# Kernel optimization log

Measured on AMD Instinct MI355X. Metric: run time of the kernel, lower is better.

## Reference

```python
import jax, jax.numpy as jnp
import numpy as np

N = 10000        # nodes
E = 160000       # edges (avg degree 16)
MUL = 128        # channel multiplicity
A = 10           # node-attr (species one-hot) dim
RAD = 8          # radial bessel features
INV_SQRT3 = 0.5773502691896258  # CG coefficient for 1o x 1o -> 0e


def _mlp(x, Ws):
    # RadialMLP: linear layers with SiLU between, no activation on last
    for W in Ws[:-1]:
        x = jax.nn.silu(x @ W)
    return x @ Ws[-1]


def setup_inputs() -> dict:
    key = jax.random.key(0)
    ks = jax.random.split(key, 25)

    def g(k, shape):
        return jax.random.normal(k, shape, jnp.float32) / np.float32(np.sqrt(shape[0]))

    return {
        "node_attrs": jax.random.uniform(ks[0], (N, A), jnp.float32),
        "node_feats": jax.random.normal(ks[1], (N, 4 * MUL), jnp.float32),
        "edge_attrs": jax.random.normal(ks[2], (E, 4), jnp.float32),
        "edge_feats": jax.random.uniform(ks[3], (E, RAD), jnp.float32),
        "W_src": g(ks[5], (A, MUL)),
        "W_tgt": g(ks[6], (A, MUL)),
        "W_up0": g(ks[7], (MUL, MUL)),
        "W_up1": g(ks[8], (MUL, MUL)),
        "W_skip0": g(ks[9], (MUL, MUL)),
        "W_skip1": g(ks[10], (MUL, MUL)),
        "W_res0": g(ks[11], (MUL, 2 * MUL)),
        "W_res1": g(ks[12], (MUL, MUL)),
        "W_lin1_0": g(ks[13], (2 * MUL, 2 * MUL)),
        "W_lin1_1": g(ks[14], (2 * MUL, MUL)),
        "W_lin2_0": g(ks[15], (MUL, MUL)),
        "W_lin2_1": g(ks[16], (MUL, MUL)),
        "W_rad1": g(ks[17], (RAD + 2 * MUL, 64)),
        "W_rad2": g(ks[18], (64, 64)),
        "W_rad3": g(ks[19], (64, 64)),
        "W_rad4": g(ks[20], (64, 4 * MUL)),
        "W_den1": g(ks[21], (RAD + 2 * MUL, 64)),
        "W_den2": g(ks[22], (64, 1)),
        "alpha": jnp.ones((), jnp.float32),   # scaled by 20 inside (alpha = param * 20)
        "beta": jnp.zeros((), jnp.float32),
        "edge_index": jax.random.randint(ks[4], (E, 2), 0, N),
    }


def _forward(node_attrs, node_feats, edge_attrs, edge_feats,
             W_src, W_tgt, W_up0, W_up1, W_skip0, W_skip1, W_res0, W_res1,
             W_lin1_0, W_lin1_1, W_lin2_0, W_lin2_1,
             W_rad1, W_rad2, W_rad3, W_rad4, W_den1, W_den2,
             alpha, beta, edge_index):
    n = node_feats.shape[0]
    # split node feats into 128x0e scalars and 128x1o vectors (mul_ir layout)
    s = node_feats[:, :MUL]                           # [N, 128]
    v = node_feats[:, MUL:].reshape(n, MUL, 3)        # [N, 128, 3]

    # skip connection: Linear(node_feats_irreps -> hidden_irreps)
    sc_s = s @ W_skip0
    sc_v = jnp.einsum("nui,uv->nvi", v, W_skip1)
    sc = jnp.concatenate([sc_s, sc_v.reshape(n, -1)], axis=-1)  # [N, 512]

    # linear_up (node_feats -> edge_irreps) and linear_res (-> irreps_nonlin)
    up_s = s @ W_up0
    up_v = jnp.einsum("nui,uv->nvi", v, W_up1)
    res_s = s @ W_res0                                # [N, 256] (scalars + gates)
    res_v = jnp.einsum("nui,uv->nvi", v, W_res1)      # [N, 128, 3]

    # per-species scalar embeddings, gathered per edge
    src_emb = node_attrs @ W_src                      # [N, 128]
    tgt_emb = node_attrs @ W_tgt
    snd = edge_index[:, 0]
    rcv = edge_index[:, 1]
    aug = jnp.concatenate([edge_feats, src_emb[snd], tgt_emb[rcv]], axis=-1)  # [E, 264]

    # radial MLP -> per-edge tensor-product weights; density MLP
    tpw = _mlp(aug, [W_rad1, W_rad2, W_rad3, W_rad4])  # [E, 512]
    edge_density = jnp.tanh(_mlp(aug, [W_den1, W_den2]) ** 2)  # [E, 1]
    density = jax.ops.segment_sum(edge_density, rcv, num_segments=n)  # [N, 1]

    # equivariant tensor product (uvu, per-edge weights), lmax=1 CG paths
    xs = up_s[snd]                                    # [E, 128]
    xv = up_v[snd]                                    # [E, 128, 3]
    y0 = edge_attrs[:, :1]                            # [E, 1]
    y1 = edge_attrs[:, 1:4]                           # [E, 3]
    wA, wB, wC, wD = jnp.split(tpw, 4, axis=-1)
    mA = wA * xs * y0                                               # 0e x 0e -> 0e
    mD = wD * jnp.einsum("eui,ei->eu", xv, y1) * INV_SQRT3          # 1o x 1o -> 0e
    mB = (wB * xs)[:, :, None] * y1[:, None, :]                     # 0e x 1o -> 1o
    mC = wC[:, :, None] * xv * y0[:, :, None]                       # 1o x 0e -> 1o
    m_s = jnp.concatenate([mA, mD], axis=-1)          # [E, 256]
    m_v = jnp.concatenate([mB, mC], axis=1)           # [E, 256, 3]

    # scatter-add messages to receiver nodes
    msg_s = jax.ops.segment_sum(m_s, rcv, num_segments=n)  # [N, 256]
    msg_v = jax.ops.segment_sum(m_v, rcv, num_segments=n)  # [N, 256, 3]

    # linear_1 (irreps_mid -> irreps_nonlin), density normalization, residual
    msg_s = msg_s @ W_lin1_0                          # [N, 256]
    msg_v = jnp.einsum("nui,uv->nvi", msg_v, W_lin1_1)  # [N, 128, 3]
    denom = density * beta + alpha * 20.0             # [N, 1]
    msg_s = msg_s / denom + res_s
    msg_v = msg_v / denom[..., None] + res_v

    # equivariant gate nonlinearity: silu on scalars, sigmoid gates on vectors
    scal = jax.nn.silu(msg_s[:, :MUL])
    gate = jax.nn.sigmoid(msg_s[:, MUL:])
    vec = msg_v * gate[:, :, None]

    # linear_2 and reshape to [N, channels, (lmax+1)^2]
    out_s = scal @ W_lin2_0                           # [N, 128]
    out_v = jnp.einsum("nui,uv->nvi", vec, W_lin2_1)  # [N, 128, 3]
    message = jnp.concatenate([out_s[:, :, None], out_v], axis=-1)  # [N, 128, 4]
    return message, sc


def reference(node_attrs, node_feats, edge_attrs, edge_feats,
              W_src, W_tgt, W_up0, W_up1, W_skip0, W_skip1, W_res0, W_res1,
              W_lin1_0, W_lin1_1, W_lin2_0, W_lin2_1,
              W_rad1, W_rad2, W_rad3, W_rad4, W_den1, W_den2,
              alpha, beta, edge_index):
    return _forward(node_attrs, node_feats, edge_attrs, edge_feats,
                    W_src, W_tgt, W_up0, W_up1, W_skip0, W_skip1, W_res0, W_res1,
                    W_lin1_0, W_lin1_1, W_lin2_0, W_lin2_1,
                    W_rad1, W_rad2, W_rad3, W_rad4, W_den1, W_den2,
                    alpha, beta, edge_index)
```

## Files before the change

kernel.cpp:

```cpp
#include <hip/hip_runtime.h>
#include <hip/hip_bf16.h>
#include <math.h>

#define NN 10000
#define NE 160000
#define MUL 128
#define ADIM 10
#define RADF 8
#define HID 64
#define INV_SQRT3 0.57735026918962576f
#define NB64 157

typedef __attribute__((ext_vector_type(8))) short bf16x8;
typedef __attribute__((ext_vector_type(4))) float f32x4;

__device__ __forceinline__ float silu_f(float x){ return x / (1.0f + __expf(-x)); }
__device__ __forceinline__ float sigmoid_f(float x){ return 1.0f / (1.0f + __expf(-x)); }
__device__ __forceinline__ unsigned short f2b(float f){
  union{float f; unsigned u;} v; v.f=f;
  unsigned r = (v.u + 0x7fffu + ((v.u>>16)&1u))>>16;
  return (unsigned short)r;
}
__device__ __forceinline__ unsigned short f2bh(float f){
  __hip_bfloat16 h = __float2bfloat16(f);
  union{ __hip_bfloat16 h; unsigned short u; } v; v.h=h; return v.u;
}
__device__ __forceinline__ unsigned f2b2(float lo, float hi){
  float2 t; t.x=lo; t.y=hi;
  __hip_bfloat162 h2 = __float22bfloat162_rn(t);
  union{ __hip_bfloat162 h; unsigned u; } v; v.h=h2; return v.u;
}
__device__ __forceinline__ float b2f(unsigned short h){
  union{unsigned u; float f;} v; v.u = ((unsigned)h)<<16; return v.f;
}
__device__ __forceinline__ float b2f_lo(unsigned u){
  union{unsigned u; float f;} v; v.u = u<<16; return v.f;
}
__device__ __forceinline__ float b2f_hi(unsigned u){
  union{unsigned u; float f;} v; v.u = u & 0xffff0000u; return v.f;
}

__global__ __launch_bounds__(256) void k_nodeemb(
    const float* __restrict__ attrs, const float* __restrict__ Wc,
    float* __restrict__ pA, float* __restrict__ pB){
  int idx = blockIdx.x*256 + threadIdx.x;
  if (idx >= NN*64) return;
  int n = idx>>6, c = idx&63;
  float s0=0,s1=0,s2=0,s3=0;
  #pragma unroll
  for (int a=0;a<ADIM;a++){
    float x = attrs[n*ADIM+a];
    s0 += x*Wc[(0*ADIM+a)*64+c];
    s1 += x*Wc[(1*ADIM+a)*64+c];
    s2 += x*Wc[(2*ADIM+a)*64+c];
    s3 += x*Wc[(3*ADIM+a)*64+c];
  }
  pA[(size_t)n*128 + c*2 + 0] = s0;
  pA[(size_t)n*128 + c*2 + 1] = s2;
  pB[(size_t)n*128 + c*2 + 0] = s1;
  pB[(size_t)n*128 + c*2 + 1] = s3;
}

__global__ __launch_bounds__(256) void k_feat_prep(
    const float* __restrict__ feats, unsigned short* __restrict__ fs16,
    unsigned short* __restrict__ fv16){
  int idx = blockIdx.x*256 + threadIdx.x;
  int n = idx >> 9, c = idx & 511;
  float v = feats[idx];
  if (c < 128) fs16[n*128 + c] = f2bh(v);
  else {
    int q = c - 128; int u = q/3; int i = q - 3*u;
    fv16[((size_t)n*3 + i)*128 + u] = f2bh(v);
  }
}

__global__ __launch_bounds__(256) void k_prep(
    const float* __restrict__ Wr2, const float* __restrict__ Wr3,
    const float* __restrict__ Wr4,
    const float* __restrict__ Wl10, const float* __restrict__ Wl11,
    const float* __restrict__ Wl20, const float* __restrict__ Wl21,
    const float* __restrict__ Wsk0, const float* __restrict__ Wup0, const float* __restrict__ Wres0,
    const float* __restrict__ Wsk1, const float* __restrict__ Wup1, const float* __restrict__ Wres1,
    const float* __restrict__ Wsrc, const float* __restrict__ Wtgt,
    const float* __restrict__ Wr1, const float* __restrict__ Wd1,
    unsigned short* __restrict__ WTr2, unsigned short* __restrict__ WTr3,
    unsigned short* __restrict__ WTr4,
    unsigned short* __restrict__ Wl10T, unsigned short* __restrict__ Wl11T,
    unsigned short* __restrict__ Wl20T, unsigned short* __restrict__ Wl21T,
    unsigned short* __restrict__ WnsT, unsigned short* __restrict__ WnvT,
    float* __restrict__ Wc){
  int idx = blockIdx.x*256 + threadIdx.x;
  if (idx < 4096){
    int j = idx; int n=j>>6, k=j&63;
    WTr2[j] = f2b(Wr2[k*64+n]);
  } else if (idx < 8192){
    int j = idx-4096; int n=j>>6, k=j&63;
    WTr3[j] = f2b(Wr3[k*64+n]);
  } else if (idx < 40960){
    int j = idx-8192; int n=j>>6, k=j&63;
    WTr4[j] = f2b(Wr4[k*512+n]);
  } else if (idx < 106496){
    int j = idx-40960; int n=j>>8, k=j&255;
    Wl10T[j] = f2b(Wl10[k*256+n]);
  } else if (idx < 139264){
    int j = idx-106496; int n=j>>8, k=j&255;
    Wl11T[j] = f2b(Wl11[k*128+n]);
  } else if (idx < 155648){
    int j = idx-139264; int n=j>>7, k=j&127;
    Wl20T[j] = f2b(Wl20[k*128+n]);
  } else if (idx < 172032){
    int j = idx-155648; int n=j>>7, k=j&127;
    Wl21T[j] = f2b(Wl21[k*128+n]);
  } else if (idx < 237568){
    int j = idx-172032; int n=j>>7, k=j&127;
    float v;
    if (n < 128)      v = Wsk0[k*128+n];
    else if (n < 256) v = Wup0[k*128+(n-128)];
    else              v = Wres0[k*256+(n-256)];
    WnsT[j] = f2b(v);
  } else if (idx < 286720){
    int j = idx-237568; int n=j>>7, k=j&127;
    float v;
    if (n < 128)      v = Wsk1[k*128+n];
    else if (n < 256) v = Wup1[k*128+(n-128)];
    else              v = Wres1[k*128+(n-256)];
    WnvT[j] = f2b(v);
  } else if (idx < 286976){
    int j = idx - 286720;
    int m = j>>6, c = j&63;
    const float* WA = (m&1)? Wtgt : Wsrc;
    const float* WB = (m<2)? Wr1 : Wd1;
    int koff = (m&1)? 136 : 8;
    for (int a=0;a<ADIM;a++){
      float s=0.f;
      for (int k=0;k<128;k++) s += WA[a*128+k]*WB[(koff+k)*64+c];
      Wc[(m*ADIM+a)*64+c] = s;
    }
  }
}

__global__ __launch_bounds__(256) void k_node_pre2(
    const unsigned short* __restrict__ fs16, const unsigned short* __restrict__ fv16,
    const unsigned short* __restrict__ WnsT, const unsigned short* __restrict__ WnvT,
    float* __restrict__ out_sc,
    unsigned short* __restrict__ upk16,
    float* __restrict__ res_s, float* __restrict__ res_v){
  __shared__ unsigned short fA[64][136];
  int nb = blockIdx.x*64;
  int c = blockIdx.y;
  int g, ntc;
  if (c < 4){ g=0; ntc=c; } else { g = 1 + (c-4)/3; ntc = (c-4)%3; }
  int tid = threadIdx.x;
  int w = tid>>6, l = tid&63, m0 = w*16, lr = l&15, lg = l>>4;
  for (int idx=tid; idx<64*16; idx+=256){
    int row = idx>>4, s8 = idx&15;
    int n = min(nb+row, NN-1);
    const unsigned short* src = (g==0) ? &fs16[(size_t)n*128 + s8*8]
                                       : &fv16[((size_t)n*3 + (g-1))*128 + s8*8];
    *(uint4*)&fA[row][s8*8] = *(const uint4*)src;
  }
  __syncthreads();
  const unsigned short* WT = ((g==0)? WnsT : WnvT) + (size_t)ntc*128*128;
  f32x4 acc[8];
  #pragma unroll
  for (int t=0;t<8;t++) acc[t]=(f32x4)(0.f);
  #pragma unroll
  for (int kb=0;kb<4;kb++){
    bf16x8 a = *(const bf16x8*)&fA[m0+lr][kb*32 + lg*8];
    #pragma unroll
    for (int t=0;t<8;t++){
      bf16x8 b = *(const bf16x8*)&WT[(size_t)(t*16+lr)*128 + kb*32 + lg*8];
      acc[t] = __builtin_amdgcn_mfma_f32_16x16x32_bf16(a, b, acc[t], 0,0,0);
    }
  }
  #pragma unroll
  for (int t=0;t<8;t++){
    #pragma unroll
    for (int r=0;r<4;r++){
      int col = (ntc*8+t)*16 + lr;
      int row = m0 + lg*4 + r;
      int n = nb + row;
      if (n < NN){
        float v = acc[t][r];
        if (g==0){
          if (col < 128)      out_sc[(size_t)n*512 + col] = v;
          else if (col < 256){
            int cc = col-128;
            upk16[(size_t)n*512 + (cc&63)*8 + (cc>>6)] = f2bh(v);
          } else              res_s[(size_t)n*256 + col-256] = v;
        } else {
          int i = g-1;
          if (col < 128)      out_sc[(size_t)n*512 + 128 + col*3 + i] = v;
          else if (col < 256){
            int cc = col-128;
            upk16[(size_t)n*512 + (cc&63)*8 + (1+i)*2 + (cc>>6)] = f2bh(v);
          } else              res_v[((size_t)n*3+i)*128 + col-256] = v;
        }
      }
    }
  }
}

__global__ __launch_bounds__(256) void k_deg(const int* __restrict__ eidx, int* __restrict__ deg){
  int i = blockIdx.x*256+threadIdx.x;
  if (i<NE) atomicAdd(&deg[eidx[2*i+1]],1);
}
__global__ __launch_bounds__(256) void k_scan(const int* __restrict__ deg, int* __restrict__ offsets){
  __shared__ int part[256];
  int t = threadIdx.x; int base = t*40;
  int s=0;
  for (int k=0;k<40;k++){ int idx=base+k; if (idx<NN) s+=deg[idx]; }
  part[t]=s; __syncthreads();
  if (t==0){ int run=0; for (int i=0;i<256;i++){ int v=part[i]; part[i]=run; run+=v; } }
  __syncthreads();
  int run = part[t];
  for (int k=0;k<40;k++){
    int idx=base+k;
    if (idx<=NN) offsets[idx]=run;
    if (idx<NN) run+=deg[idx];
  }
}
__global__ __launch_bounds__(256) void k_fill(const int* __restrict__ eidx, const int* __restrict__ offsets,
                                              int* __restrict__ cursor, int* __restrict__ elist){
  int i = blockIdx.x*256+threadIdx.x;
  if (i<NE){ int r = eidx[2*i+1]; int p = atomicAdd(&cursor[r],1); elist[offsets[r]+p]=i; }
}

__global__ __launch_bounds__(256) void k_tpw(
    const int* __restrict__ elist, const int* __restrict__ eidx,
    const float* __restrict__ ef, const float* __restrict__ ea,
    const float* __restrict__ pA, const float* __restrict__ pB,
    const float* __restrict__ Wr1, const float* __restrict__ Wd1, const float* __restrict__ Wd2,
    const unsigned short* __restrict__ WTr2, const unsigned short* __restrict__ WTr3,
    const unsigned short* __restrict__ WTr4,
    const int* __restrict__ offsets, int nstart, int nend, int cap,
    unsigned* __restrict__ tpwp, float4* __restrict__ ybuf,
    int* __restrict__ sndbuf, float* __restrict__ densbuf){
  __shared__ unsigned short hA[64][72];
  __shared__ unsigned short hB[64][72];
  __shared__ float efs[64][8];
  __shared__ int s_snd[64], s_rcv[64];
  int ebase = offsets[nstart];
  int eend  = min(offsets[nend], ebase + cap);
  int i0 = ebase + blockIdx.x*64;
  if (i0 >= eend) return;
  int nrows = min(64, eend - i0);
  int tid = threadIdx.x;
  int w = tid>>6, l = tid&63, m0 = w*16, lr = l&15, lg = l>>4;
  if (tid < 64){
    int ii = min(i0 + tid, eend-1);
    int e = elist[ii];
    int sn = eidx[2*e], rc = eidx[2*e+1];
    s_snd[tid]=sn; s_rcv[tid]=rc;
    if (tid < nrows){
      int li = i0 - ebase + tid;
      sndbuf[li] = sn;
      ybuf[li] = ((const float4*)ea)[e];
    }
  }
  if (tid < 128){
    int r = tid>>1, hf = tid&1;
    int e = elist[min(i0+r, eend-1)];
    *(float4*)&efs[r][hf*4] = *(const float4*)&ef[(size_t)e*8 + hf*4];
  }
  __syncthreads();
  {
    float wr[8], wd[8];
    #pragma unroll
    for (int k=0;k<8;k++){ wr[k]=Wr1[k*64+l]; wd[k]=Wd1[k*64+l]; }
    float wd2c = Wd2[l];
    #pragma unroll
    for (int j=0;j<16;j++){
      int r = m0+j;
      int sn = s_snd[r], rc = s_rcv[r];
      float2 av = *(const float2*)&pA[(size_t)sn*128 + l*2];
      float2 bv = *(const float2*)&pB[(size_t)rc*128 + l*2];
      float h  = av.x + bv.x;
      float hd = av.y + bv.y;
      #pragma unroll
      for (int k=0;k<8;k++){ float ek=efs[r][k]; h += ek*wr[k]; hd += ek*wd[k]; }
      hA[r][l] = f2bh(silu_f(h));
      float sv = silu_f(hd)*wd2c;
      #pragma unroll
      for (int m=32;m;m>>=1) sv += __shfl_xor(sv, m);
      if (l==0 && r < nrows) densbuf[i0 - ebase + r] = tanhf(sv*sv);
    }
  }
  f32x4 acc[4];
  #pragma unroll
  for (int nt=0;nt<4;nt++) acc[nt]=(f32x4)(0.f);
  #pragma unroll
  for (int kb=0;kb<2;kb++){
    bf16x8 a = *(const bf16x8*)&hA[m0+lr][kb*32 + lg*8];
    #pragma unroll
    for (int nt=0;nt<4;nt++){
      bf16x8 b = *(const bf16x8*)&WTr2[(nt*16+lr)*64 + kb*32 + lg*8];
      acc[nt] = __builtin_amdgcn_mfma_f32_16x16x32_bf16(a, b, acc[nt], 0,0,0);
    }
  }
  #pragma unroll
  for (int nt=0;nt<4;nt++)
    #pragma unroll
    for (int r=0;r<4;r++)
      hB[m0+lg*4+r][nt*16+lr] = f2bh(silu_f(acc[nt][r]));
  #pragma unroll
  for (int nt=0;nt<4;nt++) acc[nt]=(f32x4)(0.f);
  #pragma unroll
  for (int kb=0;kb<2;kb++){
    bf16x8 a = *(const bf16x8*)&hB[m0+lr][kb*32 + lg*8];
    #pragma unroll
    for (int nt=0;nt<4;nt++){
      bf16x8 b = *(const bf16x8*)&WTr3[(nt*16+lr)*64 + kb*32 + lg*8];
      acc[nt] = __builtin_amdgcn_mfma_f32_16x16x32_bf16(a, b, acc[nt], 0,0,0);
    }
  }
  #pragma unroll
  for (int nt=0;nt<4;nt++)
    #pragma unroll
    for (int r=0;r<4;r++)
      hA[m0+lg*4+r][nt*16+lr] = f2bh(silu_f(acc[nt][r]));
  int erow0 = i0 - ebase;
  #pragma unroll
  for (int nt=0; nt<4; nt++){
    unsigned pvv[4][4];
    #pragma unroll
    for (int G=0; G<4; G++){
      f32x4 aE=(f32x4)(0.f), aO=(f32x4)(0.f);
      #pragma unroll
      for (int kb=0; kb<2; kb++){
        bf16x8 a  = *(const bf16x8*)&hA[m0+lr][kb*32 + lg*8];
        bf16x8 bE = *(const bf16x8*)&WTr4[((2*G)*64+nt*16+lr)*64 + kb*32 + lg*8];
        bf16x8 bO = *(const bf16x8*)&WTr4[((2*G+1)*64+nt*16+lr)*64 + kb*32 + lg*8];
        aE = __builtin_amdgcn_mfma_f32_16x16x32_bf16(a, bE, aE, 0,0,0);
        aO = __builtin_amdgcn_mfma_f32_16x16x32_bf16(a, bO, aO, 0,0,0);
      }
      #pragma unroll
      for (int r=0;r<4;r++)
        pvv[r][G] = f2b2(aE[r], aO[r]);
    }
    #pragma unroll
    for (int r=0;r<4;r++){
      int row = m0 + lg*4 + r;
      if (row < nrows)
        *(uint4*)&tpwp[(size_t)(erow0+row)*256 + (nt*16+lr)*4] = *(uint4*)&pvv[r][0];
    }
  }
}

__global__ __launch_bounds__(256) void k_gather(
    const unsigned* __restrict__ tpwp, const float4* __restrict__ ybuf,
    const int* __restrict__ sndbuf, const float* __restrict__ densbuf,
    const uint4* __restrict__ upk4,
    const int* __restrict__ offsets, int nstart,
    unsigned short* __restrict__ msg_s16, unsigned short* __restrict__ msg_v16,
    float* __restrict__ density){
  __shared__ float part[2][1024];
  __shared__ float pden[2];
  int w = threadIdx.x>>6, l = threadIdx.x&63;
  int pairIdx = w>>1, half = w&1;
  int n = nstart + blockIdx.x*2 + pairIdx;
  int ebase = offsets[nstart];
  int s0 = offsets[n], s1 = offsets[n+1];
  float mA0=0,mA1=0,mD0=0,mD1=0;
  float mB00=0,mB01=0,mB10=0,mB11=0,mB20=0,mB21=0;
  float mC00=0,mC01=0,mC10=0,mC11=0,mC20=0,mC21=0;
  float dsum=0;
  for (int i=s0+half; i<s1; i+=2){
    int li = i - ebase;
    int sn = sndbuf[li];
    float4 y = ybuf[li];
    dsum += densbuf[li];
    uint4 tq = *(const uint4*)&tpwp[(size_t)li*256 + l*4];
    uint4 uq = upk4[(size_t)sn*64 + l];
    float wA0=b2f_lo(tq.x), wA1=b2f_hi(tq.x);
    float wB0=b2f_lo(tq.y), wB1=b2f_hi(tq.y);
    float wC0=b2f_lo(tq.z), wC1=b2f_hi(tq.z);
    float wD0=b2f_lo(tq.w), wD1=b2f_hi(tq.w);
    float xs0=b2f_lo(uq.x), xs1=b2f_hi(uq.x);
    float xv00=b2f_lo(uq.y), xv01=b2f_hi(uq.y);
    float xv10=b2f_lo(uq.z), xv11=b2f_hi(uq.z);
    float xv20=b2f_lo(uq.w), xv21=b2f_hi(uq.w);
    mA0 += wA0*xs0*y.x; mA1 += wA1*xs1*y.x;
    float dot0 = xv00*y.y + xv10*y.z + xv20*y.w;
    float dot1 = xv01*y.y + xv11*y.z + xv21*y.w;
    mD0 += wD0*dot0; mD1 += wD1*dot1;
    float b0 = wB0*xs0, b1 = wB1*xs1;
    mB00 += b0*y.y; mB01 += b1*y.y;
    mB10 += b0*y.z; mB11 += b1*y.z;
    mB20 += b0*y.w; mB21 += b1*y.w;
    float c0 = wC0*y.x, c1 = wC1*y.x;
    mC00 += c0*xv00; mC01 += c1*xv01;
    mC10 += c0*xv10; mC11 += c1*xv11;
    mC20 += c0*xv20; mC21 += c1*xv21;
  }
  if (half==1){
    float* P = part[pairIdx];
    P[0*64+l]=mA0;  P[1*64+l]=mA1;  P[2*64+l]=mD0;  P[3*64+l]=mD1;
    P[4*64+l]=mB00; P[5*64+l]=mB01; P[6*64+l]=mB10; P[7*64+l]=mB11;
    P[8*64+l]=mB20; P[9*64+l]=mB21; P[10*64+l]=mC00; P[11*64+l]=mC01;
    P[12*64+l]=mC10; P[13*64+l]=mC11; P[14*64+l]=mC20; P[15*64+l]=mC21;
    if (l==0) pden[pairIdx]=dsum;
  }
  __syncthreads();
  if (half==0){
    const float* P = part[pairIdx];
    mA0+=P[0*64+l];  mA1+=P[1*64+l];  mD0+=P[2*64+l];  mD1+=P[3*64+l];
    mB00+=P[4*64+l]; mB01+=P[5*64+l]; mB10+=P[6*64+l]; mB11+=P[7*64+l];
    mB20+=P[8*64+l]; mB21+=P[9*64+l]; mC00+=P[10*64+l]; mC01+=P[11*64+l];
    mC10+=P[12*64+l]; mC11+=P[13*64+l]; mC20+=P[14*64+l]; mC21+=P[15*64+l];
    dsum += pden[pairIdx];
    unsigned short* ms = msg_s16 + (size_t)n*256;
    ms[l]=f2bh(mA0); ms[64+l]=f2bh(mA1);
    ms[128+l]=f2bh(mD0*INV_SQRT3); ms[192+l]=f2bh(mD1*INV_SQRT3);
    unsigned short* mv = msg_v16 + (size_t)n*768;
    mv[l]=f2bh(mB00);     mv[64+l]=f2bh(mB01);  mv[128+l]=f2bh(mC00); mv[192+l]=f2bh(mC01);
    mv[256+l]=f2bh(mB10); mv[320+l]=f2bh(mB11); mv[384+l]=f2bh(mC10); mv[448+l]=f2bh(mC11);
    mv[512+l]=f2bh(mB20); mv[576+l]=f2bh(mB21); mv[640+l]=f2bh(mC20); mv[704+l]=f2bh(mC21);
    if (l==0) density[n]=dsum;
  }
}

__global__ __launch_bounds__(256) void k_post1(
    const unsigned short* __restrict__ msg_s16, const unsigned short* __restrict__ msg_v16,
    const float* __restrict__ density,
    const float* __restrict__ res_s, const float* __restrict__ res_v,
    const unsigned short* __restrict__ Wl10T, const unsigned short* __restrict__ Wl11T,
    const float* __restrict__ alphap, const float* __restrict__ betap,
    unsigned short* __restrict__ scal16, unsigned short* __restrict__ gate16,
    unsigned short* __restrict__ vtmp16){
  __shared__ unsigned short sm[64][264];
  __shared__ float sden[64];
  int nb = blockIdx.x*64, y = blockIdx.y;
  int tid = threadIdx.x;
  int w = tid>>6, l = tid&63, m0 = w*16, lr = l&15, lg = l>>4;
  for (int idx=tid; idx<64*32; idx+=256){
    int row = idx>>5, s8 = idx&31;
    int n = min(nb+row, NN-1);
    const unsigned short* src = (y<2)? &msg_s16[(size_t)n*256 + s8*8]
                                     : &msg_v16[(size_t)n*768 + (y-2)*256 + s8*8];
    *(uint4*)&sm[row][s8*8] = *(const uint4*)src;
  }
  if (tid < 64){
    int n = min(nb+tid, NN-1);
    sden[tid] = density[n]*betap[0] + alphap[0]*20.0f;
  }
  __syncthreads();
  const unsigned short* BT = (y<2)? (Wl10T + (size_t)y*128*256) : Wl11T;
  f32x4 acc[8];
  #pragma unroll
  for (int t=0;t<8;t++) acc[t]=(f32x4)(0.f);
  for (int kb=0;kb<8;kb++){
    bf16x8 a = *(const bf16x8*)&sm[m0+lr][kb*32 + lg*8];
    #pragma unroll
    for (int t=0;t<8;t++){
      bf16x8 b = *(const bf16x8*)&BT[(size_t)(t*16+lr)*256 + kb*32 + lg*8];
      acc[t] = __builtin_amdgcn_mfma_f32_16x16x32_bf16(a, b, acc[t], 0,0,0);
    }
  }
  #pragma unroll
  for (int t=0;t<8;t++){
    #pragma unroll
    for (int r=0;r<4;r++){
      int col = t*16+lr;
      int row = m0 + lg*4 + r;
      int n = nb + row;
      if (n < NN){
        float v = acc[t][r]/sden[row];
        if (y==0){
          v += res_s[(size_t)n*256 + col];
          scal16[(size_t)n*128 + col] = f2bh(silu_f(v));
        } else if (y==1){
          v += res_s[(size_t)n*256 + 128 + col];
          gate16[(size_t)n*128 + col] = f2bh(sigmoid_f(v));
        } else {
          int i = y-2;
          v += res_v[((size_t)n*3+i)*128 + col];
          vtmp16[((size_t)i*NN + n)*128 + col] = f2bh(v);
        }
      }
    }
  }
}

__global__ __launch_bounds__(256) void k_post2(
    const unsigned short* __restrict__ scal16, const unsigned short* __restrict__ gate16,
    const unsigned short* __restrict__ vtmp16,
    const unsigned short* __restrict__ Wl20T, const unsigned short* __restrict__ Wl21T,
    float* __restrict__ out_msg){
  __shared__ unsigned short sA[64][136];
  int nb = blockIdx.x*64, y = blockIdx.y;
  int tid = threadIdx.x;
  int w = tid>>6, l = tid&63, m0 = w*16, lr = l&15, lg = l>>4;
  for (int idx=tid; idx<64*16; idx+=256){
    int row = idx>>4, s8 = idx&15;
    int n = min(nb+row, NN-1);
    if (y==0){
      *(uint4*)&sA[row][s8*8] = *(const uint4*)&scal16[(size_t)n*128 + s8*8];
    } else {
      int i = y-1;
      uint4 va = *(const uint4*)&vtmp16[((size_t)i*NN + n)*128 + s8*8];
      uint4 vg = *(const uint4*)&gate16[(size_t)n*128 + s8*8];
      const unsigned short* pa = (const unsigned short*)&va;
      const unsigned short* pg = (const unsigned short*)&vg;
      unsigned short o[8];
      #pragma unroll
      for (int j=0;j<8;j++) o[j] = f2bh(b2f(pa[j])*b2f(pg[j]));
      *(uint4*)&sA[row][s8*8] = *(const uint4*)o;
    }
  }
  __syncthreads();
  const unsigned short* BT = (y==0)? Wl20T : Wl21T;
  f32x4 acc[8];
  #pragma unroll
  for (int t=0;t<8;t++) acc[t]=(f32x4)(0.f);
  #pragma unroll
  for (int kb=0;kb<4;kb++){
    bf16x8 a = *(const bf16x8*)&sA[m0+lr][kb*32 + lg*8];
    #pragma unroll
    for (int t=0;t<8;t++){
      bf16x8 b = *(const bf16x8*)&BT[(size_t)(t*16+lr)*128 + kb*32 + lg*8];
      acc[t] = __builtin_amdgcn_mfma_f32_16x16x32_bf16(a, b, acc[t], 0,0,0);
    }
  }
  #pragma unroll
  for (int t=0;t<8;t++){
    #pragma unroll
    for (int r=0;r<4;r++){
      int col = t*16+lr;
      int n = nb + m0 + lg*4 + r;
      if (n < NN) out_msg[(size_t)n*512 + col*4 + y] = acc[t][r];
    }
  }
}

extern "C" void kernel_launch(void* const* d_in, const int* in_sizes, int n_in,
                              void* d_out, int out_size, void* d_ws, size_t ws_size,
                              hipStream_t stream){
  (void)in_sizes; (void)n_in; (void)out_size;
  const float* attrs = (const float*)d_in[0];
  const float* feats = (const float*)d_in[1];
  const float* ea    = (const float*)d_in[2];
  const float* ef    = (const float*)d_in[3];
  const float* Wsrc  = (const float*)d_in[4];
  const float* Wtgt  = (const float*)d_in[5];
  const float* Wup0  = (const float*)d_in[6];
  const float* Wup1  = (const float*)d_in[7];
  const float* Wsk0  = (const float*)d_in[8];
  const float* Wsk1  = (const float*)d_in[9];
  const float* Wres0 = (const float*)d_in[10];
  const float* Wres1 = (const float*)d_in[11];
  const float* Wl10  = (const float*)d_in[12];
  const float* Wl11  = (const float*)d_in[13];
  const float* Wl20  = (const float*)d_in[14];
  const float* Wl21  = (const float*)d_in[15];
  const float* Wr1   = (const float*)d_in[16];
  const float* Wr2   = (const float*)d_in[17];
  const float* Wr3   = (const float*)d_in[18];
  const float* Wr4   = (const float*)d_in[19];
  const float* Wd1   = (const float*)d_in[20];
  const float* Wd2   = (const float*)d_in[21];
  const float* alphap= (const float*)d_in[22];
  const float* betap = (const float*)d_in[23];
  const int*   eidx  = (const int*)d_in[24];

  const size_t fixed_bytes =
      (size_t)NN*(512 + 1536 + 1024 + 1536 + 4 + 1024 + 256 + 768 + 512 + 512 + 256) +
      (size_t)286976*2 + 4*ADIM*64*4 +
      (10240+10240+10256)*4 + (size_t)NE*4 + 64*256;
  int nchunk, npc, cap;
  if (fixed_bytes + (size_t)NE*1048 + 65536 <= ws_size){ nchunk=1; npc=NN;   cap=NE;    }
  else if (fixed_bytes + 81920ULL*1048 + 65536 <= ws_size){ nchunk=2; npc=5000; cap=81920; }
  else { nchunk=4; npc=2500; cap=44032; }

  char* p = (char*)d_ws;
  auto alloc = [&](size_t bytes)->char*{ char* r=p; p += (bytes+255)&~(size_t)255; return r; };
  unsigned* tpwp  = (unsigned*)alloc((size_t)cap*256*4);
  unsigned short* msg_s16 = (unsigned short*)alloc((size_t)NN*256*2);
  unsigned short* msg_v16 = (unsigned short*)alloc((size_t)NN*768*2);
  float*  res_s   = (float*)alloc((size_t)NN*256*4);
  float*  res_v   = (float*)alloc((size_t)NN*384*4);
  float*  density = (float*)alloc((size_t)NN*4);
  float4* ybuf    = (float4*)alloc((size_t)cap*16);
  float*  densbuf = (float*)alloc((size_t)cap*4);
  int*    sndbuf  = (int*)alloc((size_t)cap*4);
  uint4*  upk     = (uint4*)alloc((size_t)NN*64*16);
  unsigned short* fs16 = (unsigned short*)alloc((size_t)NN*128*2);
  unsigned short* fv16 = (unsigned short*)alloc((size_t)NN*384*2);
  float* pA = (float*)alloc((size_t)NN*128*4);
  float* pB = (float*)alloc((size_t)NN*128*4);
  float* Wc  = (float*)alloc(4*ADIM*64*4);
  unsigned short* gate16 = (unsigned short*)alloc((size_t)NN*128*2);
  unsigned short* WTr2 = (unsigned short*)alloc(4096*2);
  unsigned short* WTr3 = (unsigned short*)alloc(4096*2);
  unsigned short* WTr4 = (unsigned short*)alloc(32768*2);
  unsigned short* Wl10T = (unsigned short*)alloc(65536*2);
  unsigned short* Wl11T = (unsigned short*)alloc(32768*2);
  unsigned short* Wl20T = (unsigned short*)alloc(16384*2);
  unsigned short* Wl21T = (unsigned short*)alloc(16384*2);
  unsigned short* WnsT  = (unsigned short*)alloc(65536*2);
  unsigned short* WnvT  = (unsigned short*)alloc(49152*2);
  int* deg     = (int*)alloc(10240*4);
  int* cursor  = (int*)alloc(10240*4);
  int* offsets = (int*)alloc(10256*4);
  int* elist   = (int*)alloc((size_t)NE*4);

  unsigned short* scal16 = fs16;
  unsigned short* vtmp16 = fv16;

  float* out_msg = (float*)d_out;
  float* out_sc  = out_msg + (size_t)NN*512;

  hipMemsetAsync(deg, 0, 2*10240*sizeof(int), stream);

  k_prep<<<1121, 256, 0, stream>>>(Wr2, Wr3, Wr4, Wl10, Wl11, Wl20, Wl21,
                                   Wsk0, Wup0, Wres0, Wsk1, Wup1, Wres1,
                                   Wsrc, Wtgt, Wr1, Wd1,
                                   WTr2, WTr3, WTr4,
                                   Wl10T, Wl11T, Wl20T, Wl21T, WnsT, WnvT, Wc);
  k_nodeemb<<<(NN*64+255)/256, 256, 0, stream>>>(attrs, Wc, pA, pB);
  k_feat_prep<<<NN*512/256, 256, 0, stream>>>(feats, fs16, fv16);
  k_node_pre2<<<dim3(NB64,13), 256, 0, stream>>>(fs16, fv16, WnsT, WnvT,
                                                 out_sc, (unsigned short*)upk, res_s, res_v);
  k_deg<<<(NE+255)/256, 256, 0, stream>>>(eidx, deg);
  k_scan<<<1, 256, 0, stream>>>(deg, offsets);
  k_fill<<<(NE+255)/256, 256, 0, stream>>>(eidx, offsets, cursor, elist);

  int tpw_blocks = (cap+63)/64;
  for (int c=0; c<nchunk; ++c){
    k_tpw<<<tpw_blocks, 256, 0, stream>>>(elist, eidx, ef, ea, pA, pB,
                                          Wr1, Wd1, Wd2, WTr2, WTr3, WTr4,
                                          offsets, c*npc, (c+1)*npc, cap,
                                          tpwp, ybuf, sndbuf, densbuf);
    k_gather<<<npc/2, 256, 0, stream>>>(tpwp, ybuf, sndbuf, densbuf, upk,
                                        offsets, c*npc, msg_s16, msg_v16, density);
  }

  k_post1<<<dim3(NB64,5), 256, 0, stream>>>(msg_s16, msg_v16, density, res_s, res_v,
                                            Wl10T, Wl11T, alphap, betap,
                                            scal16, gate16, vtmp16);
  k_post2<<<dim3(NB64,4), 256, 0, stream>>>(scal16, gate16, vtmp16,
                                            Wl20T, Wl21T, out_msg);
}
```

Before: 440.5 us.

## Scatter edge data into receiver-sorted buffers in fill and drop the elist indirection

k_fill now writes sender, receiver, edge attrs and radial features directly into receiver-sorted buffers instead of writing only an edge permutation list. k_tpw then reads those contiguous buffers. It broadcasts per-row metadata and features with wavefront shuffles instead of staging them in LDS behind a block barrier. This removes the double-indirect random gathers from k_tpw, at the cost of scattered multi-field writes in k_fill and extra workspace sized to the full edge count.

After: 442.9 us. No clear change (+0.5%).

```diff
diff --git a/kernel.cpp b/kernel.cpp
--- a/kernel.cpp
+++ b/kernel.cpp
@@ -220,26 +220,33 @@
     if (idx<NN) run+=deg[idx];
   }
 }
-__global__ __launch_bounds__(256) void k_fill(const int* __restrict__ eidx, const int* __restrict__ offsets,
-                                              int* __restrict__ cursor, int* __restrict__ elist){
+__global__ __launch_bounds__(256) void k_fill(
+    const int* __restrict__ eidx, const float* __restrict__ ef, const float* __restrict__ ea,
+    const int* __restrict__ offsets, int* __restrict__ cursor,
+    int* __restrict__ sndbuf, int* __restrict__ rcvbuf,
+    float4* __restrict__ ybuf, float* __restrict__ efb){
   int i = blockIdx.x*256+threadIdx.x;
-  if (i<NE){ int r = eidx[2*i+1]; int p = atomicAdd(&cursor[r],1); elist[offsets[r]+p]=i; }
+  if (i<NE){
+    int sn = eidx[2*i], rc = eidx[2*i+1];
+    int p = offsets[rc] + atomicAdd(&cursor[rc],1);
+    sndbuf[p]=sn; rcvbuf[p]=rc;
+    ybuf[p] = ((const float4*)ea)[i];
+    *(float4*)&efb[(size_t)p*8]     = *(const float4*)&ef[(size_t)i*8];
+    *(float4*)&efb[(size_t)p*8 + 4] = *(const float4*)&ef[(size_t)i*8 + 4];
+  }
 }
 
 __global__ __launch_bounds__(256) void k_tpw(
-    const int* __restrict__ elist, const int* __restrict__ eidx,
-    const float* __restrict__ ef, const float* __restrict__ ea,
+    const int* __restrict__ sndbuf, const int* __restrict__ rcvbuf,
+    const float* __restrict__ efb,
     const float* __restrict__ pA, const float* __restrict__ pB,
     const float* __restrict__ Wr1, const float* __restrict__ Wd1, const float* __restrict__ Wd2,
     const unsigned short* __restrict__ WTr2, const unsigned short* __restrict__ WTr3,
     const unsigned short* __restrict__ WTr4,
     const int* __restrict__ offsets, int nstart, int nend, int cap,
-    unsigned* __restrict__ tpwp, float4* __restrict__ ybuf,
-    int* __restrict__ sndbuf, float* __restrict__ densbuf){
+    unsigned* __restrict__ tpwp, float* __restrict__ densbuf){
   __shared__ unsigned short hA[64][72];
   __shared__ unsigned short hB[64][72];
-  __shared__ float efs[64][8];
-  __shared__ int s_snd[64], s_rcv[64];
   int ebase = offsets[nstart];
   int eend  = min(offsets[nend], ebase + cap);
   int i0 = ebase + blockIdx.x*64;
@@ -247,23 +254,19 @@
   int nrows = min(64, eend - i0);
   int tid = threadIdx.x;
   int w = tid>>6, l = tid&63, m0 = w*16, lr = l&15, lg = l>>4;
-  if (tid < 64){
-    int ii = min(i0 + tid, eend-1);
-    int e = elist[ii];
-    int sn = eidx[2*e], rc = eidx[2*e+1];
-    s_snd[tid]=sn; s_rcv[tid]=rc;
-    if (tid < nrows){
-      int li = i0 - ebase + tid;
-      sndbuf[li] = sn;
-      ybuf[li] = ((const float4*)ea)[e];
-    }
-  }
-  if (tid < 128){
-    int r = tid>>1, hf = tid&1;
-    int e = elist[min(i0+r, eend-1)];
-    *(float4*)&efs[r][hf*4] = *(const float4*)&ef[(size_t)e*8 + hf*4];
-  }
-  __syncthreads();
+  int wbase = i0 + m0;
+  int v_meta = 0;
+  {
+    int pos = min(wbase + (l&15), eend-1);
+    if (l < 16)      v_meta = sndbuf[pos];
+    else if (l < 32) v_meta = rcvbuf[pos];
+  }
+  float ra, rb;
+  {
+    int pos = min(wbase + (l&15), eend-1);
+    ra = efb[(size_t)pos*8 + (l>>4)];
+    rb = efb[(size_t)pos*8 + 4 + (l>>4)];
+  }
   {
     float wr[8], wd[8];
     #pragma unroll
@@ -271,19 +274,21 @@
     float wd2c = Wd2[l];
     #pragma unroll
     for (int j=0;j<16;j++){
-      int r = m0+j;
-      int sn = s_snd[r], rc = s_rcv[r];
+      int sn = __shfl(v_meta, j);
+      int rc = __shfl(v_meta, 16+j);
       float2 av = *(const float2*)&pA[(size_t)sn*128 + l*2];
       float2 bv = *(const float2*)&pB[(size_t)rc*128 + l*2];
+      float e0=__shfl(ra,j),    e1=__shfl(ra,16+j), e2=__shfl(ra,32+j), e3=__shfl(ra,48+j);
+      float e4=__shfl(rb,j),    e5=__shfl(rb,16+j), e6=__shfl(rb,32+j), e7=__shfl(rb,48+j);
       float h  = av.x + bv.x;
       float hd = av.y + bv.y;
-      #pragma unroll
-      for (int k=0;k<8;k++){ float ek=efs[r][k]; h += ek*wr[k]; hd += ek*wd[k]; }
-      hA[r][l] = f2bh(silu_f(h));
+      h  += e0*wr[0]+e1*wr[1]+e2*wr[2]+e3*wr[3]+e4*wr[4]+e5*wr[5]+e6*wr[6]+e7*wr[7];
+      hd += e0*wd[0]+e1*wd[1]+e2*wd[2]+e3*wd[3]+e4*wd[4]+e5*wd[5]+e6*wd[6]+e7*wd[7];
+      hA[m0+j][l] = f2bh(silu_f(h));
       float sv = silu_f(hd)*wd2c;
       #pragma unroll
       for (int m=32;m;m>>=1) sv += __shfl_xor(sv, m);
-      if (l==0 && r < nrows) densbuf[i0 - ebase + r] = tanhf(sv*sv);
+      if (l==0 && m0+j < nrows) densbuf[wbase + j] = tanhf(sv*sv);
     }
   }
   f32x4 acc[4];
@@ -367,9 +372,9 @@
   float dsum=0;
   for (int i=s0+half; i<s1; i+=2){
     int li = i - ebase;
-    int sn = sndbuf[li];
-    float4 y = ybuf[li];
-    dsum += densbuf[li];
+    int sn = sndbuf[i];
+    float4 y = ybuf[i];
+    dsum += densbuf[i];
     uint4 tq = *(const uint4*)&tpwp[(size_t)li*256 + l*4];
     uint4 uq = upk4[(size_t)sn*64 + l];
     float wA0=b2f_lo(tq.x), wA1=b2f_hi(tq.x);
@@ -565,11 +570,12 @@
 
   const size_t fixed_bytes =
       (size_t)NN*(512 + 1536 + 1024 + 1536 + 4 + 1024 + 256 + 768 + 512 + 512 + 256) +
+      (size_t)NE*60 +
       (size_t)286976*2 + 4*ADIM*64*4 +
-      (10240+10240+10256)*4 + (size_t)NE*4 + 64*256;
+      (10240+10240+10256)*4 + 64*256;
   int nchunk, npc, cap;
-  if (fixed_bytes + (size_t)NE*1048 + 65536 <= ws_size){ nchunk=1; npc=NN;   cap=NE;    }
-  else if (fixed_bytes + 81920ULL*1048 + 65536 <= ws_size){ nchunk=2; npc=5000; cap=81920; }
+  if (fixed_bytes + (size_t)NE*1024 + 65536 <= ws_size){ nchunk=1; npc=NN;   cap=NE;    }
+  else if (fixed_bytes + 81920ULL*1024 + 65536 <= ws_size){ nchunk=2; npc=5000; cap=81920; }
   else { nchunk=4; npc=2500; cap=44032; }
 
   char* p = (char*)d_ws;
@@ -580,9 +586,11 @@
   float*  res_s   = (float*)alloc((size_t)NN*256*4);
   float*  res_v   = (float*)alloc((size_t)NN*384*4);
   float*  density = (float*)alloc((size_t)NN*4);
-  float4* ybuf    = (float4*)alloc((size_t)cap*16);
-  float*  densbuf = (float*)alloc((size_t)cap*4);
-  int*    sndbuf  = (int*)alloc((size_t)cap*4);
+  float4* ybuf    = (float4*)alloc((size_t)NE*16);
+  float*  densbuf = (float*)alloc((size_t)NE*4);
+  int*    sndbuf  = (int*)alloc((size_t)NE*4);
+  int*    rcvbuf  = (int*)alloc((size_t)NE*4);
+  float*  efb     = (float*)alloc((size_t)NE*32);
   uint4*  upk     = (uint4*)alloc((size_t)NN*64*16);
   unsigned short* fs16 = (unsigned short*)alloc((size_t)NN*128*2);
   unsigned short* fv16 = (unsigned short*)alloc((size_t)NN*384*2);
@@ -602,7 +610,6 @@
   int* deg     = (int*)alloc(10240*4);
   int* cursor  = (int*)alloc(10240*4);
   int* offsets = (int*)alloc(10256*4);
-  int* elist   = (int*)alloc((size_t)NE*4);
 
   unsigned short* scal16 = fs16;
   unsigned short* vtmp16 = fv16;
@@ -623,14 +630,15 @@
                                                  out_sc, (unsigned short*)upk, res_s, res_v);
   k_deg<<<(NE+255)/256, 256, 0, stream>>>(eidx, deg);
   k_scan<<<1, 256, 0, stream>>>(deg, offsets);
-  k_fill<<<(NE+255)/256, 256, 0, stream>>>(eidx, offsets, cursor, elist);
+  k_fill<<<(NE+255)/256, 256, 0, stream>>>(eidx, ef, ea, offsets, cursor,
+                                           sndbuf, rcvbuf, ybuf, efb);
 
   int tpw_blocks = (cap+63)/64;
   for (int c=0; c<nchunk; ++c){
-    k_tpw<<<tpw_blocks, 256, 0, stream>>>(elist, eidx, ef, ea, pA, pB,
+    k_tpw<<<tpw_blocks, 256, 0, stream>>>(sndbuf, rcvbuf, efb, pA, pB,
                                           Wr1, Wd1, Wd2, WTr2, WTr3, WTr4,
                                           offsets, c*npc, (c+1)*npc, cap,
-                                          tpwp, ybuf, sndbuf, densbuf);
+                                          tpwp, densbuf);
     k_gather<<<npc/2, 256, 0, stream>>>(tpwp, ybuf, sndbuf, densbuf, upk,
                                         offsets, c*npc, msg_s16, msg_v16, density);
   }
```
